# Optimization experiments

Measured on AMD Instinct MI355X. Metric: run time of the kernel, lower is better.

The kernel has to match this reference:

```python
import jax, jax.numpy as jnp
import numpy as np

TOTAL_WORDS = 10000
EMBED = 100
SEQ = 80
UNITS = 64
BATCH = 4096


def setup_inputs() -> dict:
    key = jax.random.key(0)
    ks = jax.random.split(key, 8)
    tokens = jax.random.randint(ks[0], (BATCH, SEQ), 0, TOTAL_WORDS)
    emb = jax.random.normal(ks[1], (TOTAL_WORDS, EMBED), jnp.float32) * 0.05
    W1 = jax.random.normal(ks[2], (EMBED, UNITS), jnp.float32) * (1.0 / np.sqrt(EMBED))
    U1 = jax.random.normal(ks[3], (UNITS, UNITS), jnp.float32) * (1.0 / np.sqrt(UNITS))
    b1 = jnp.zeros((UNITS,), jnp.float32)
    W2 = jax.random.normal(ks[4], (UNITS, UNITS), jnp.float32) * (1.0 / np.sqrt(UNITS))
    U2 = jax.random.normal(ks[5], (UNITS, UNITS), jnp.float32) * (1.0 / np.sqrt(UNITS))
    b2 = jnp.zeros((UNITS,), jnp.float32)
    Wo = jax.random.normal(ks[6], (UNITS, 1), jnp.float32) * (1.0 / np.sqrt(UNITS))
    bo = jnp.zeros((1,), jnp.float32)
    return {"tokens": tokens, "emb": emb, "W1": W1, "U1": U1, "b1": b1,
            "W2": W2, "U2": U2, "b2": b2, "Wo": Wo, "bo": bo}


def reference(tokens, emb, W1, U1, b1, W2, U2, b2, Wo, bo):
    # Embedding lookup: [B, T, E]
    x = emb[tokens]
    # Precompute input projections for layer 1 across all timesteps: [B, T, U]
    xw1 = jnp.einsum('bte,eu->btu', x, W1) + b1
    B = tokens.shape[0]
    h0 = jnp.zeros((B, UNITS), xw1.dtype)

    def step(carry, inp):
        h1, h2 = carry
        h1 = jnp.tanh(inp + h1 @ U1)                 # SimpleRNN layer 1
        h2 = jnp.tanh(h1 @ W2 + b2 + h2 @ U2)        # SimpleRNN layer 2 consumes layer-1 seq
        return (h1, h2), None

    (_, h2), _ = jax.lax.scan(step, (h0, h0), jnp.swapaxes(xw1, 0, 1))
    # Dense(1) head + sigmoid: [B, 1]
    return jax.nn.sigmoid(h2 @ Wo + bo)
```

## Files before the change

### kernel.cpp

```cpp
#include <hip/hip_runtime.h>

#define BATCH 4096
#define SEQ   80
#define EMBED 100
#define UNITS 64
#define NTILE (BATCH / 16)
#define NVOC  10000
#define NVWV  ((NVOC + 15) / 16)
#define NPAIR2 (SEQ / 2)

typedef float f32x4  __attribute__((ext_vector_type(4)));
typedef short bf16x8 __attribute__((ext_vector_type(8)));

#define MFMA16 __builtin_amdgcn_mfma_f32_16x16x32_bf16

#define TAB_OFF 0u
#define W1T_OFF 1280000u
#define U1T_OFF 1296384u
#define W2T_OFF 1304576u
#define U2T_OFF 1312768u
#define XW2_OFF 1320960u

__device__ __forceinline__ unsigned f2bfu(float f) {
    union { float f; unsigned u; } x; x.f = f;
    return (x.u + 0x7fffu + ((x.u >> 16) & 1u)) >> 16;
}
__device__ __forceinline__ unsigned cvtpk(float lo, float hi) {
    unsigned r;
    asm("v_cvt_pk_bf16_f32 %0, %1, %2" : "=v"(r) : "v"(lo), "v"(hi));
    return r;
}
__device__ __forceinline__ float bflo(unsigned u) {
    union { unsigned u; float f; } x; x.u = u << 16; return x.f;
}
__device__ __forceinline__ float bfhi(unsigned u) {
    union { unsigned u; float f; } x; x.u = u & 0xffff0000u; return x.f;
}
__device__ __forceinline__ float fast_tanh(float x) {
    float e = __builtin_amdgcn_exp2f(x * 2.8853900817779268f);
    float r = __builtin_amdgcn_rcpf(e + 1.0f);
    return __builtin_fmaf(-2.0f, r, 1.0f);
}

__global__ __launch_bounds__(256) void miniprep_kernel(
    const float* __restrict__ W1, const float* __restrict__ U1,
    const float* __restrict__ W2, const float* __restrict__ U2,
    char* __restrict__ ws)
{
    ushort* w1t = (ushort*)(ws + W1T_OFF);
    ushort* u1t = (ushort*)(ws + U1T_OFF);
    ushort* w2t = (ushort*)(ws + W2T_OFF);
    ushort* u2t = (ushort*)(ws + U2T_OFF);
    const int i = blockIdx.x * 256 + threadIdx.x;
    if (i < 8192) {
        const int u = i >> 7, k = i & 127;
        w1t[i] = (k < EMBED) ? (ushort)f2bfu(W1[k * UNITS + u]) : (ushort)0;
    } else if (i < 12288) {
        const int j = i - 8192, u = j >> 6, k = j & 63;
        u1t[j] = (ushort)f2bfu(U1[k * UNITS + u]);
    } else if (i < 16384) {
        const int j = i - 12288, u = j >> 6, k = j & 63;
        w2t[j] = (ushort)f2bfu(W2[k * UNITS + u]);
    } else if (i < 20480) {
        const int j = i - 16384, u = j >> 6, k = j & 63;
        u2t[j] = (ushort)f2bfu(U2[k * UNITS + u]);
    }
}

__global__ __launch_bounds__(256) void tableproj_kernel(
    const float* __restrict__ emb,
    const float* __restrict__ b1,
    const ushort* __restrict__ w1t,
    char* __restrict__ table)
{
    const int lane = threadIdx.x & 63;
    const int wid  = threadIdx.x >> 6;
    const int gw   = blockIdx.x * 4 + wid;
    if (gw >= NVWV) return;
    const int m15  = lane & 15;
    const int kgrp = lane >> 4;
    const int v    = gw * 16 + m15;
    const int vc   = v < NVOC ? v : NVOC - 1;

    bf16x8 aW1[4][4];
    #pragma unroll
    for (int mt = 0; mt < 4; ++mt)
        #pragma unroll
        for (int ks = 0; ks < 4; ++ks)
            aW1[mt][ks] = *(const bf16x8*)(w1t + (16 * mt + m15) * 128 + kgrp * 8 + 32 * ks);

    const float* rp = emb + (size_t)vc * EMBED;
    bf16x8 bf[4];
    #pragma unroll
    for (int ks = 0; ks < 3; ++ks) {
        f32x4 e0 = *(const f32x4*)(rp + kgrp * 8 + 32 * ks);
        f32x4 e1 = *(const f32x4*)(rp + kgrp * 8 + 32 * ks + 4);
        uint4 u;
        u.x = cvtpk(e0.x, e0.y); u.y = cvtpk(e0.z, e0.w);
        u.z = cvtpk(e1.x, e1.y); u.w = cvtpk(e1.z, e1.w);
        bf[ks] = *(bf16x8*)&u;
    }
    {
        uint4 u = {0u, 0u, 0u, 0u};
        if (kgrp == 0) {
            f32x4 e0 = *(const f32x4*)(rp + 96);
            u.x = cvtpk(e0.x, e0.y); u.y = cvtpk(e0.z, e0.w);
        }
        bf[3] = *(bf16x8*)&u;
    }

    f32x4 acc[4];
    #pragma unroll
    for (int mt = 0; mt < 4; ++mt)
        acc[mt] = *(const f32x4*)(b1 + 16 * mt + 4 * kgrp);
    #pragma unroll
    for (int ks = 0; ks < 4; ++ks)
        #pragma unroll
        for (int mt = 0; mt < 4; ++mt)
            acc[mt] = MFMA16(aW1[mt][ks], bf[ks], acc[mt], 0, 0, 0);

    #pragma unroll
    for (int mt = 0; mt < 4; ++mt) {
        uint2 q;
        q.x = cvtpk(acc[mt][0], acc[mt][1]);
        q.y = cvtpk(acc[mt][2], acc[mt][3]);
        *(uint2*)(table + (size_t)v * 128 + mt * 32 + kgrp * 8) = q;
    }
}

__global__ __launch_bounds__(256) void expand_kernel(
    const int*   __restrict__ tokens,
    const uint2* __restrict__ table,
    uint4*       __restrict__ xw2)
{
    __shared__ int tokL[16][84];

    const int lane = threadIdx.x & 63;
    const int w    = threadIdx.x >> 6;
    const int m15  = lane & 15;
    const int kgrp = lane >> 4;
    const int tile = blockIdx.x;

    for (int i = threadIdx.x; i < 16 * SEQ; i += 256) {
        const int r = i / SEQ;
        const int t = i - r * SEQ;
        tokL[r][t] = tokens[(size_t)(tile * 16 + r) * SEQ + t];
    }
    __syncthreads();

    const uint2* tabp = table + w * 4 + kgrp;
    uint4* outp = xw2 + ((size_t)(tile * 4 + w)) * NPAIR2 * 64 + lane;

    #pragma unroll 4
    for (int pk = 0; pk < NPAIR2; ++pk) {
        const int tokE = tokL[m15][2 * pk];
        const int tokO = tokL[m15][2 * pk + 1];
        uint2 gE = tabp[(size_t)tokE * 16];
        uint2 gO = tabp[(size_t)tokO * 16];
        uint4 o; o.x = gE.x; o.y = gE.y; o.z = gO.x; o.w = gO.y;
        outp[(size_t)pk * 64] = o;
    }
}

__global__ __launch_bounds__(256, 1) void rnn_kernel(
    const uint4*  __restrict__ xw2,
    const ushort* __restrict__ u1t,
    const ushort* __restrict__ w2t,
    const ushort* __restrict__ u2t,
    const float*  __restrict__ b2,
    const float*  __restrict__ Wo,
    const float*  __restrict__ bo,
    float*        __restrict__ out)
{
    __shared__ __align__(16) char h1L[2][2048];
    __shared__ __align__(16) char h2L[2][2048];
    __shared__ float headp[4][16];

    const int lane = threadIdx.x & 63;
    const int w    = threadIdx.x >> 6;
    const int m15  = lane & 15;
    const int kgrp = lane >> 4;
    const int swz  = (m15 & 7) << 4;
    const int wg   = blockIdx.x;

    {
        uint4 z = {0u, 0u, 0u, 0u};
        if (threadIdx.x < 128) ((uint4*)h2L[0])[threadIdx.x] = z;
    }

    const int urow = 16 * w + m15;
    bf16x8 aU1[2], aW2[2], aU2[2];
    #pragma unroll
    for (int ks = 0; ks < 2; ++ks) {
        aU1[ks] = *(const bf16x8*)(u1t + urow * 64 + kgrp * 8 + 32 * ks);
        aW2[ks] = *(const bf16x8*)(w2t + urow * 64 + kgrp * 8 + 32 * ks);
        aU2[ks] = *(const bf16x8*)(u2t + urow * 64 + kgrp * 8 + 32 * ks);
    }
    const int ubase = 16 * w + 4 * kgrp;
    const f32x4 b2c = *(const f32x4*)(b2 + ubase);

    const uint4* xwp = xw2 + ((size_t)(wg * 4 + w)) * NPAIR2 * 64 + lane;
    uint4 r0 = xwp[0];
    uint4 r1 = xwp[64];
    uint4 r2 = xwp[2 * 64];

    {
        float t0 = fast_tanh(bflo(r0.x)), t1 = fast_tanh(bfhi(r0.x));
        float t2 = fast_tanh(bflo(r0.y)), t3 = fast_tanh(bfhi(r0.y));
        uint2 pk; pk.x = cvtpk(t0, t1); pk.y = cvtpk(t2, t3);
        *(uint2*)(h1L[0] + m15 * 128 + ((32 * w + 8 * kgrp) ^ swz)) = pk;
    }
    asm volatile("s_waitcnt lgkmcnt(0)" ::: "memory");
    __builtin_amdgcn_s_barrier();

    float d2f0 = 0.f, d2f1 = 0.f, d2f2 = 0.f, d2f3 = 0.f;

#define LBAR() do { asm volatile("s_waitcnt lgkmcnt(0)" ::: "memory"); \
                    __builtin_amdgcn_s_barrier(); } while (0)
#define PHASE(QX, QY, P, Q)                                                      \
  {                                                                              \
    bf16x8 bh1a = *(const bf16x8*)(h1L[P] + m15 * 128 + ((kgrp * 16     ) ^ swz)); \
    bf16x8 bh1b = *(const bf16x8*)(h1L[P] + m15 * 128 + ((kgrp * 16 + 64) ^ swz)); \
    bf16x8 bh2a = *(const bf16x8*)(h2L[P] + m15 * 128 + ((kgrp * 16     ) ^ swz)); \
    bf16x8 bh2b = *(const bf16x8*)(h2L[P] + m15 * 128 + ((kgrp * 16 + 64) ^ swz)); \
    f32x4 d1 = {bflo(QX), bfhi(QX), bflo(QY), bfhi(QY)};                         \
    d1 = MFMA16(aU1[0], bh1a, d1, 0, 0, 0);                                      \
    d1 = MFMA16(aU1[1], bh1b, d1, 0, 0, 0);                                      \
    f32x4 dC = b2c;                                                              \
    dC = MFMA16(aW2[0], bh1a, dC, 0, 0, 0);                                      \
    dC = MFMA16(aW2[1], bh1b, dC, 0, 0, 0);                                      \
    f32x4 dD = {0.f, 0.f, 0.f, 0.f};                                             \
    dD = MFMA16(aU2[0], bh2a, dD, 0, 0, 0);                                      \
    dD = MFMA16(aU2[1], bh2b, dD, 0, 0, 0);                                      \
    float n0 = fast_tanh(d1[0]);                                                 \
    float n1 = fast_tanh(d1[1]);                                                 \
    float n2 = fast_tanh(d1[2]);                                                 \
    float n3 = fast_tanh(d1[3]);                                                 \
    d2f0 = fast_tanh(dC[0] + dD[0]);                                             \
    d2f1 = fast_tanh(dC[1] + dD[1]);                                             \
    d2f2 = fast_tanh(dC[2] + dD[2]);                                             \
    d2f3 = fast_tanh(dC[3] + dD[3]);                                             \
    {                                                                            \
        uint2 pk; pk.x = cvtpk(n0, n1); pk.y = cvtpk(n2, n3);                    \
        *(uint2*)(h1L[Q] + m15 * 128 + ((32 * w + 8 * kgrp) ^ swz)) = pk;        \
    }                                                                            \
    {                                                                            \
        uint2 pk; pk.x = cvtpk(d2f0, d2f1); pk.y = cvtpk(d2f2, d2f3);            \
        *(uint2*)(h2L[Q] + m15 * 128 + ((32 * w + 8 * kgrp) ^ swz)) = pk;        \
    }                                                                            \
    LBAR();                                                                      \
  }

    for (int k = 0; k < NPAIR2; ++k) {
        const int pn = (k + 3 < NPAIR2) ? k + 3 : NPAIR2 - 1;
        uint4 r3 = xwp[(size_t)pn * 64];
        PHASE(r0.z, r0.w, 0, 1)
        PHASE(r1.x, r1.y, 1, 0)
        r0 = r1; r1 = r2; r2 = r3;
    }
#undef PHASE
#undef LBAR

    const f32x4 woc = *(const f32x4*)(Wo + ubase);
    float p = d2f0 * woc[0] + d2f1 * woc[1] + d2f2 * woc[2] + d2f3 * woc[3];
    p += __shfl_xor(p, 16, 64);
    p += __shfl_xor(p, 32, 64);
    if (lane < 16) headp[w][lane] = p;
    __syncthreads();
    if (threadIdx.x < 16) {
        const float z = headp[0][threadIdx.x] + headp[1][threadIdx.x]
                      + headp[2][threadIdx.x] + headp[3][threadIdx.x] + bo[0];
        const float e = __builtin_amdgcn_exp2f(-z * 1.4426950408889634f);
        out[wg * 16 + threadIdx.x] = __builtin_amdgcn_rcpf(1.0f + e);
    }
}

extern "C" void kernel_launch(void* const* d_in, const int* in_sizes, int n_in,
                              void* d_out, int out_size, void* d_ws, size_t ws_size,
                              hipStream_t stream) {
    const int*   tokens = (const int*)  d_in[0];
    const float* emb    = (const float*)d_in[1];
    const float* W1     = (const float*)d_in[2];
    const float* U1     = (const float*)d_in[3];
    const float* b1     = (const float*)d_in[4];
    const float* W2     = (const float*)d_in[5];
    const float* U2     = (const float*)d_in[6];
    const float* b2     = (const float*)d_in[7];
    const float* Wo     = (const float*)d_in[8];
    const float* bo     = (const float*)d_in[9];
    float* out = (float*)d_out;
    char*  ws  = (char*)d_ws;

    miniprep_kernel<<<80, 256, 0, stream>>>(W1, U1, W2, U2, ws);
    tableproj_kernel<<<(NVWV + 3) / 4, 256, 0, stream>>>(
        emb, b1, (const ushort*)(ws + W1T_OFF), ws + TAB_OFF);
    expand_kernel<<<NTILE, 256, 0, stream>>>(
        tokens, (const uint2*)(ws + TAB_OFF), (uint4*)(ws + XW2_OFF));
    rnn_kernel<<<NTILE, 256, 0, stream>>>(
        (const uint4*)(ws + XW2_OFF),
        (const ushort*)(ws + U1T_OFF), (const ushort*)(ws + W2T_OFF),
        (const ushort*)(ws + U2T_OFF),
        b2, Wo, bo, out);
}
```

Before: 56.70 us.

## Drop weight-prep kernel, convert weights in-kernel, split expand across more waves

Removes the separate miniprep launch that transposed and converted W1/U1/W2/U2 to bf16. The tableproj and rnn kernels now gather fp32 weights directly with strided scalar loads and convert them in registers. The expand kernel no longer stages tokens in LDS and has each wave handle half the timesteps, launching 512 blocks instead of 256. This saves one launch and a barrier but adds many uncoalesced scalar weight loads in each block's prologue.

After: 58.87 us. +3.8%, slower.

```diff
diff --git a/kernel.cpp b/kernel.cpp
--- a/kernel.cpp
+++ b/kernel.cpp
@@ -15,11 +15,7 @@
 #define MFMA16 __builtin_amdgcn_mfma_f32_16x16x32_bf16
 
 #define TAB_OFF 0u
-#define W1T_OFF 1280000u
-#define U1T_OFF 1296384u
-#define W2T_OFF 1304576u
-#define U2T_OFF 1312768u
-#define XW2_OFF 1320960u
+#define XW2_OFF 1280000u
 
 __device__ __forceinline__ unsigned f2bfu(float f) {
     union { float f; unsigned u; } x; x.f = f;
@@ -42,35 +38,10 @@
     return __builtin_fmaf(-2.0f, r, 1.0f);
 }
 
-__global__ __launch_bounds__(256) void miniprep_kernel(
-    const float* __restrict__ W1, const float* __restrict__ U1,
-    const float* __restrict__ W2, const float* __restrict__ U2,
-    char* __restrict__ ws)
-{
-    ushort* w1t = (ushort*)(ws + W1T_OFF);
-    ushort* u1t = (ushort*)(ws + U1T_OFF);
-    ushort* w2t = (ushort*)(ws + W2T_OFF);
-    ushort* u2t = (ushort*)(ws + U2T_OFF);
-    const int i = blockIdx.x * 256 + threadIdx.x;
-    if (i < 8192) {
-        const int u = i >> 7, k = i & 127;
-        w1t[i] = (k < EMBED) ? (ushort)f2bfu(W1[k * UNITS + u]) : (ushort)0;
-    } else if (i < 12288) {
-        const int j = i - 8192, u = j >> 6, k = j & 63;
-        u1t[j] = (ushort)f2bfu(U1[k * UNITS + u]);
-    } else if (i < 16384) {
-        const int j = i - 12288, u = j >> 6, k = j & 63;
-        w2t[j] = (ushort)f2bfu(W2[k * UNITS + u]);
-    } else if (i < 20480) {
-        const int j = i - 16384, u = j >> 6, k = j & 63;
-        u2t[j] = (ushort)f2bfu(U2[k * UNITS + u]);
-    }
-}
-
 __global__ __launch_bounds__(256) void tableproj_kernel(
     const float* __restrict__ emb,
     const float* __restrict__ b1,
-    const ushort* __restrict__ w1t,
+    const float* __restrict__ W1,
     char* __restrict__ table)
 {
     const int lane = threadIdx.x & 63;
@@ -84,10 +55,17 @@
 
     bf16x8 aW1[4][4];
     #pragma unroll
-    for (int mt = 0; mt < 4; ++mt)
+    for (int mt = 0; mt < 4; ++mt) {
+        const int u = 16 * mt + m15;
         #pragma unroll
         for (int ks = 0; ks < 4; ++ks)
-            aW1[mt][ks] = *(const bf16x8*)(w1t + (16 * mt + m15) * 128 + kgrp * 8 + 32 * ks);
+            #pragma unroll
+            for (int j = 0; j < 8; ++j) {
+                const int k = kgrp * 8 + j + 32 * ks;
+                aW1[mt][ks][j] = (k < EMBED) ? (short)f2bfu(W1[k * UNITS + u])
+                                             : (short)0;
+            }
+    }
 
     const float* rp = emb + (size_t)vc * EMBED;
     bf16x8 bf[4];
@@ -133,28 +111,26 @@
     const uint2* __restrict__ table,
     uint4*       __restrict__ xw2)
 {
-    __shared__ int tokL[16][84];
-
     const int lane = threadIdx.x & 63;
-    const int w    = threadIdx.x >> 6;
+    const int wid  = threadIdx.x >> 6;
+    const int gwid = blockIdx.x * 4 + wid;
+    const int tile = gwid >> 3;
+    const int sub  = gwid & 7;
+    const int w    = sub >> 1;
+    const int half = sub & 1;
     const int m15  = lane & 15;
     const int kgrp = lane >> 4;
-    const int tile = blockIdx.x;
-
-    for (int i = threadIdx.x; i < 16 * SEQ; i += 256) {
-        const int r = i / SEQ;
-        const int t = i - r * SEQ;
-        tokL[r][t] = tokens[(size_t)(tile * 16 + r) * SEQ + t];
-    }
-    __syncthreads();
-
+
+    const int*   tokp = tokens + (size_t)(tile * 16 + m15) * SEQ;
     const uint2* tabp = table + w * 4 + kgrp;
     uint4* outp = xw2 + ((size_t)(tile * 4 + w)) * NPAIR2 * 64 + lane;
-
-    #pragma unroll 4
-    for (int pk = 0; pk < NPAIR2; ++pk) {
-        const int tokE = tokL[m15][2 * pk];
-        const int tokO = tokL[m15][2 * pk + 1];
+    const int pk0 = half * (NPAIR2 / 2);
+
+    #pragma unroll 5
+    for (int i = 0; i < NPAIR2 / 2; ++i) {
+        const int pk = pk0 + i;
+        const int tokE = tokp[2 * pk];
+        const int tokO = tokp[2 * pk + 1];
         uint2 gE = tabp[(size_t)tokE * 16];
         uint2 gO = tabp[(size_t)tokO * 16];
         uint4 o; o.x = gE.x; o.y = gE.y; o.z = gO.x; o.w = gO.y;
@@ -164,9 +140,9 @@
 
 __global__ __launch_bounds__(256, 1) void rnn_kernel(
     const uint4*  __restrict__ xw2,
-    const ushort* __restrict__ u1t,
-    const ushort* __restrict__ w2t,
-    const ushort* __restrict__ u2t,
+    const float*  __restrict__ U1,
+    const float*  __restrict__ W2,
+    const float*  __restrict__ U2,
     const float*  __restrict__ b2,
     const float*  __restrict__ Wo,
     const float*  __restrict__ bo,
@@ -191,11 +167,14 @@
     const int urow = 16 * w + m15;
     bf16x8 aU1[2], aW2[2], aU2[2];
     #pragma unroll
-    for (int ks = 0; ks < 2; ++ks) {
-        aU1[ks] = *(const bf16x8*)(u1t + urow * 64 + kgrp * 8 + 32 * ks);
-        aW2[ks] = *(const bf16x8*)(w2t + urow * 64 + kgrp * 8 + 32 * ks);
-        aU2[ks] = *(const bf16x8*)(u2t + urow * 64 + kgrp * 8 + 32 * ks);
-    }
+    for (int ks = 0; ks < 2; ++ks)
+        #pragma unroll
+        for (int j = 0; j < 8; ++j) {
+            const int k = kgrp * 8 + j + 32 * ks;
+            aU1[ks][j] = (short)f2bfu(U1[k * UNITS + urow]);
+            aW2[ks][j] = (short)f2bfu(W2[k * UNITS + urow]);
+            aU2[ks][j] = (short)f2bfu(U2[k * UNITS + urow]);
+        }
     const int ubase = 16 * w + 4 * kgrp;
     const f32x4 b2c = *(const f32x4*)(b2 + ubase);
 
@@ -291,14 +270,11 @@
     float* out = (float*)d_out;
     char*  ws  = (char*)d_ws;
 
-    miniprep_kernel<<<80, 256, 0, stream>>>(W1, U1, W2, U2, ws);
     tableproj_kernel<<<(NVWV + 3) / 4, 256, 0, stream>>>(
-        emb, b1, (const ushort*)(ws + W1T_OFF), ws + TAB_OFF);
-    expand_kernel<<<NTILE, 256, 0, stream>>>(
+        emb, b1, W1, ws + TAB_OFF);
+    expand_kernel<<<512, 256, 0, stream>>>(
         tokens, (const uint2*)(ws + TAB_OFF), (uint4*)(ws + XW2_OFF));
     rnn_kernel<<<NTILE, 256, 0, stream>>>(
         (const uint4*)(ws + XW2_OFF),
-        (const ushort*)(ws + U1T_OFF), (const ushort*)(ws + W2T_OFF),
-        (const ushort*)(ws + U2T_OFF),
-        b2, Wo, bo, out);
-}
+        U1, W2, U2, b2, Wo, bo, out);
+}
```
